# Performance work log

Measured on AMD Instinct MI355X. Metric: run time of the kernel, lower is better.

## Reference

```python
import jax, jax.numpy as jnp
import numpy as np

B, N, OBS, H, A = 4096, 32, 128, 64, 16

def setup_inputs() -> dict:
    key = jax.random.key(0)
    ks = jax.random.split(key, 12)
    s = 0.1  # weight scale for numerical stability
    return {
        "obs": jax.random.normal(ks[0], (B, N, OBS), jnp.float32),
        "enc_W": jax.random.normal(ks[1], (OBS, H), jnp.float32) * s,
        "enc_b": jnp.zeros((H,), jnp.float32),
        "msg_W0": jax.random.normal(ks[2], (H, H), jnp.float32) * s,
        "msg_b0": jnp.zeros((H,), jnp.float32),
        "msg_W1": jax.random.normal(ks[3], (H, H), jnp.float32) * s,
        "msg_b1": jnp.zeros((H,), jnp.float32),
        "lstm_Wx0": jax.random.normal(ks[4], (H, 4 * H), jnp.float32) * s,
        "lstm_Wh0": jax.random.normal(ks[5], (H, 4 * H), jnp.float32) * s,
        "lstm_b0": jnp.zeros((4 * H,), jnp.float32),
        "lstm_Wx1": jax.random.normal(ks[6], (H, 4 * H), jnp.float32) * s,
        "lstm_Wh1": jax.random.normal(ks[7], (H, 4 * H), jnp.float32) * s,
        "lstm_b1": jnp.zeros((4 * H,), jnp.float32),
        "act_W": jax.random.normal(ks[8], (H, A), jnp.float32) * s,
        "act_b": jnp.zeros((A,), jnp.float32),
        "val_W": jax.random.normal(ks[9], (H, 1), jnp.float32) * s,
        "val_b": jnp.zeros((1,), jnp.float32),
    }

def _lstm_cell(h, c, z, Wx, Wh, b):
    # flax OptimizedLSTMCell math: gates ordered i, f, g, o
    gates = z @ Wx + h @ Wh + b  # (BN, 4H)
    i, f, g, o = jnp.split(gates, 4, axis=-1)
    c_new = jax.nn.sigmoid(f) * c + jax.nn.sigmoid(i) * jnp.tanh(g)
    h_new = jax.nn.sigmoid(o) * jnp.tanh(c_new)
    return h_new, c_new

def reference(obs, enc_W, enc_b, msg_W0, msg_b0, msg_W1, msg_b1,
              lstm_Wx0, lstm_Wh0, lstm_b0, lstm_Wx1, lstm_Wh1, lstm_b1,
              act_W, act_b, val_W, val_b):
    b, n, _ = obs.shape
    x = jnp.tanh(obs @ enc_W + enc_b)  # (B, N, H)
    # carry=None -> zero initial state
    h_round = jnp.zeros((b, n, H), obs.dtype)
    c_round = jnp.zeros((b, n, H), obs.dtype)
    # alive_mask=None -> alive=ones(N); hard_attn=False -> no comm_action mask.
    # comm mixing matrix M[j, i] = comm_mask[j, i] * alive[j] * alive[i] / denom
    # with comm_mask = 1 - I and denom = max(num_alive - 1, 1) for 'avg' mode.
    denom = jnp.maximum(jnp.asarray(n, obs.dtype) - 1.0, 1.0)
    M = (jnp.ones((n, n), obs.dtype) - jnp.eye(n, dtype=obs.dtype)) / denom
    hop_params = [(msg_W0, msg_b0, lstm_Wx0, lstm_Wh0, lstm_b0),
                  (msg_W1, msg_b1, lstm_Wx1, lstm_Wh1, lstm_b1)]
    for (mW, mb, Wx, Wh, lb) in hop_params:
        # equivalent to broadcasting h to (B,N,N,H), masking, and summing over senders
        comm_sum = jnp.einsum('bjh,ji->bih', h_round, M)  # (B, N, H)
        msg = comm_sum @ mW + mb
        z = x + msg
        h_flat = h_round.reshape(b * n, H)
        c_flat = c_round.reshape(b * n, H)
        h_new, c_new = _lstm_cell(h_flat, c_flat, z.reshape(b * n, H), Wx, Wh, lb)
        h_round = jnp.tanh(h_new.reshape(b, n, H) + z)
        c_round = c_new.reshape(b, n, H)
    logits = h_round @ act_W + act_b           # (B, N, A)
    values = (h_round @ val_W + val_b)[..., 0]  # (B, N)
    return (logits, values, h_round, c_round)
```

## Files before the change

### kernel.cpp

```cpp
#include <hip/hip_runtime.h>
#include <hip/hip_bf16.h>

constexpr int Bn   = 4096;
constexpr int Nn   = 32;
constexpr int OBSn = 128;
constexpr int Hn   = 64;
constexpr int An   = 16;

constexpr size_t VOFF = (size_t)Bn * Nn * An;
constexpr size_t HOFF = VOFF + (size_t)Bn * Nn;
constexpr size_t COFF = HOFF + (size_t)Bn * Nn * Hn;

constexpr int T_ENC  = 0;
constexpr int T_MSG0 = 16;
constexpr int T_MSG1 = 24;
constexpr int T_WX0  = 32;
constexpr int T_WH0  = 64;
constexpr int T_WX1  = 96;
constexpr int T_WH1  = 128;
constexpr int T_ACT  = 160;
constexpr int T_TOT  = 162;

typedef short bf16x8 __attribute__((ext_vector_type(8)));
typedef float f32x4  __attribute__((ext_vector_type(4)));

union FragU { uint u[4]; uint4 q; bf16x8 v; };

__device__ __forceinline__ uint pkbf(float a, float b) {
    __hip_bfloat16 ha = __float2bfloat16(a);
    __hip_bfloat16 hb = __float2bfloat16(b);
    unsigned short ua, ub;
    __builtin_memcpy(&ua, &ha, 2);
    __builtin_memcpy(&ub, &hb, 2);
    return (uint)ua | ((uint)ub << 16);
}

__device__ __forceinline__ float rcp_(float x) {
#if __has_builtin(__builtin_amdgcn_rcpf)
    return __builtin_amdgcn_rcpf(x);
#else
    return 1.0f / x;
#endif
}
__device__ __forceinline__ float exp2_(float x) {
#if __has_builtin(__builtin_amdgcn_exp2f)
    return __builtin_amdgcn_exp2f(x);
#else
    return exp2f(x);
#endif
}
__device__ __forceinline__ float fsig(float x)  { return rcp_(1.0f + exp2_(-1.44269504f * x)); }
__device__ __forceinline__ float ftanh(float x) { return 1.0f - 2.0f * rcp_(1.0f + exp2_(2.88539008f * x)); }

__global__ void commnet_prep(
    const float* __restrict__ encW, const float* __restrict__ m0,
    const float* __restrict__ m1,   const float* __restrict__ wx0,
    const float* __restrict__ wh0,  const float* __restrict__ wx1,
    const float* __restrict__ wh1,  const float* __restrict__ aw,
    uint4* __restrict__ ws)
{
    int gid = blockIdx.x * 256 + threadIdx.x;
    if (gid >= T_TOT * 64) return;
    int tile = gid >> 6, lane = gid & 63;

    const float* W; int N, nt, kt, lt;
    if      (tile < T_MSG0) { W = encW; N = 64;  lt = tile;        nt = lt >> 2; kt = lt & 3; }
    else if (tile < T_MSG1) { W = m0;   N = 64;  lt = tile - T_MSG0; nt = lt >> 1; kt = lt & 1; }
    else if (tile < T_WX0 ) { W = m1;   N = 64;  lt = tile - T_MSG1; nt = lt >> 1; kt = lt & 1; }
    else if (tile < T_WH0 ) { W = wx0;  N = 256; lt = tile - T_WX0;  nt = lt >> 1; kt = lt & 1; }
    else if (tile < T_WX1 ) { W = wh0;  N = 256; lt = tile - T_WH0;  nt = lt >> 1; kt = lt & 1; }
    else if (tile < T_WH1 ) { W = wx1;  N = 256; lt = tile - T_WX1;  nt = lt >> 1; kt = lt & 1; }
    else if (tile < T_ACT ) { W = wh1;  N = 256; lt = tile - T_WH1;  nt = lt >> 1; kt = lt & 1; }
    else                    { W = aw;   N = 16;  lt = tile - T_ACT;  nt = 0;       kt = lt;     }

    int col = nt * 16 + (lane & 15);
    int kb  = kt * 32 + (lane >> 4) * 4;
    uint4 d;
    {
        int k0 = kb;
        d.x = pkbf(W[(k0 + 0) * N + col], W[(k0 + 1) * N + col]);
        d.y = pkbf(W[(k0 + 2) * N + col], W[(k0 + 3) * N + col]);
        k0 = kb + 16;
        d.z = pkbf(W[(k0 + 0) * N + col], W[(k0 + 1) * N + col]);
        d.w = pkbf(W[(k0 + 2) * N + col], W[(k0 + 3) * N + col]);
    }
    ws[(size_t)tile * 64 + lane] = d;
}

__device__ __forceinline__ int sidx(int row, int col) {
    return row * 64 + (col ^ ((row & 7) << 2));
}

__device__ __forceinline__ void write_cd(float* sb, const float v[2][4][4], int lane) {
    const int m = lane & 15, g = lane >> 4;
    #pragma unroll
    for (int rt = 0; rt < 2; ++rt)
        #pragma unroll
        for (int nt = 0; nt < 4; ++nt)
            #pragma unroll
            for (int r = 0; r < 4; ++r)
                sb[sidx(rt * 16 + g * 4 + r, nt * 16 + m)] = v[rt][nt][r];
}

__device__ __forceinline__ void read_af(const float* sb, int lane, FragU af[2][2]) {
    const int m = lane & 15, g = lane >> 4;
    #pragma unroll
    for (int rt = 0; rt < 2; ++rt)
        #pragma unroll
        for (int kt = 0; kt < 2; ++kt)
            #pragma unroll
            for (int h = 0; h < 2; ++h) {
                const float4 x = *(const float4*)&sb[sidx(rt * 16 + m, kt * 32 + h * 16 + g * 4)];
                af[rt][kt].u[2 * h]     = pkbf(x.x, x.y);
                af[rt][kt].u[2 * h + 1] = pkbf(x.z, x.w);
            }
}

template<bool WITHH>
__device__ __forceinline__ void gate_mm(const uint4* __restrict__ wsQ, int wxBase, int whBase,
                                        int gate, const FragU az[2][2], const FragU ah[2][2],
                                        const float* __restrict__ lb, int lane,
                                        float outv[2][4][4])
{
    const int m = lane & 15;
    #pragma unroll
    for (int nt = 0; nt < 4; ++nt) {
        f32x4 a0 = {0.f, 0.f, 0.f, 0.f};
        f32x4 a1 = {0.f, 0.f, 0.f, 0.f};
        const int ntg = gate * 4 + nt;
        #pragma unroll
        for (int kt = 0; kt < 2; ++kt) {
            FragU bw; bw.q = wsQ[(size_t)(wxBase + ntg * 2 + kt) * 64 + lane];
            a0 = __builtin_amdgcn_mfma_f32_16x16x32_bf16(az[0][kt].v, bw.v, a0, 0, 0, 0);
            a1 = __builtin_amdgcn_mfma_f32_16x16x32_bf16(az[1][kt].v, bw.v, a1, 0, 0, 0);
        }
        if (WITHH) {
            #pragma unroll
            for (int kt = 0; kt < 2; ++kt) {
                FragU bw; bw.q = wsQ[(size_t)(whBase + ntg * 2 + kt) * 64 + lane];
                a0 = __builtin_amdgcn_mfma_f32_16x16x32_bf16(ah[0][kt].v, bw.v, a0, 0, 0, 0);
                a1 = __builtin_amdgcn_mfma_f32_16x16x32_bf16(ah[1][kt].v, bw.v, a1, 0, 0, 0);
            }
        }
        const float lbv = lb[gate * 64 + nt * 16 + m];
        #pragma unroll
        for (int r = 0; r < 4; ++r) {
            outv[0][nt][r] = a0[r] + lbv;
            outv[1][nt][r] = a1[r] + lbv;
        }
    }
}

#define FORALL \
    _Pragma("unroll") for (int rt = 0; rt < 2; ++rt) \
    _Pragma("unroll") for (int nt = 0; nt < 4; ++nt) \
    _Pragma("unroll") for (int r = 0; r < 4; ++r)

__global__ __launch_bounds__(256, 2) void commnet_main(
    const float* __restrict__ obs, const uint4* __restrict__ wsQ,
    const float* __restrict__ enc_b,
    const float* __restrict__ msg_b0, const float* __restrict__ msg_b1,
    const float* __restrict__ lstm_b0, const float* __restrict__ lstm_b1,
    const float* __restrict__ act_b,
    const float* __restrict__ val_W, const float* __restrict__ val_b,
    float* __restrict__ out)
{
    __shared__ __align__(16) float sball[4 * 2048];
    const int t = threadIdx.x;
    const int wid = t >> 6, lane = t & 63;
    const int m = lane & 15, g = lane >> 4;
    float* sb = sball + wid * 2048;
    const int b = blockIdx.x * 4 + wid;

    FragU aob[2][4];
    const float* ob = obs + (size_t)b * (Nn * OBSn);
    #pragma unroll
    for (int rt = 0; rt < 2; ++rt)
        #pragma unroll
        for (int kt = 0; kt < 4; ++kt)
            #pragma unroll
            for (int h = 0; h < 2; ++h) {
                const float4 vv = *(const float4*)&ob[(rt * 16 + m) * OBSn + kt * 32 + h * 16 + g * 4];
                aob[rt][kt].u[2 * h]     = pkbf(vv.x, vv.y);
                aob[rt][kt].u[2 * h + 1] = pkbf(vv.z, vv.w);
            }
    float xv[2][4][4];
    #pragma unroll
    for (int nt = 0; nt < 4; ++nt) {
        f32x4 a0 = {0.f, 0.f, 0.f, 0.f};
        f32x4 a1 = {0.f, 0.f, 0.f, 0.f};
        #pragma unroll
        for (int kt = 0; kt < 4; ++kt) {
            FragU bw; bw.q = wsQ[(size_t)(T_ENC + nt * 4 + kt) * 64 + lane];
            a0 = __builtin_amdgcn_mfma_f32_16x16x32_bf16(aob[0][kt].v, bw.v, a0, 0, 0, 0);
            a1 = __builtin_amdgcn_mfma_f32_16x16x32_bf16(aob[1][kt].v, bw.v, a1, 0, 0, 0);
        }
        const float eb = enc_b[nt * 16 + m];
        #pragma unroll
        for (int r = 0; r < 4; ++r) {
            xv[0][nt][r] = ftanh(a0[r] + eb);
            xv[1][nt][r] = ftanh(a1[r] + eb);
        }
    }

    float zv[2][4][4], cv[2][4][4], hv[2][4][4], tg[2][4][4], si[2][4][4];
    FragU az[2][2], ah[2][2];

    #pragma unroll
    for (int nt = 0; nt < 4; ++nt) {
        const float mb = msg_b0[nt * 16 + m];
        #pragma unroll
        for (int rt = 0; rt < 2; ++rt)
            #pragma unroll
            for (int r = 0; r < 4; ++r)
                zv[rt][nt][r] = xv[rt][nt][r] + mb;
    }
    write_cd(sb, zv, lane);
    read_af(sb, lane, az);

    gate_mm<false>(wsQ, T_WX0, 0, 0, az, az, lstm_b0, lane, tg);
    FORALL { si[rt][nt][r] = fsig(tg[rt][nt][r]); }
    gate_mm<false>(wsQ, T_WX0, 0, 2, az, az, lstm_b0, lane, tg);
    FORALL { cv[rt][nt][r] = si[rt][nt][r] * ftanh(tg[rt][nt][r]); }
    gate_mm<false>(wsQ, T_WX0, 0, 3, az, az, lstm_b0, lane, tg);
    FORALL { hv[rt][nt][r] = ftanh(fsig(tg[rt][nt][r]) * ftanh(cv[rt][nt][r]) + zv[rt][nt][r]); }

    {
        float cm[2][4][4];
        #pragma unroll
        for (int nt = 0; nt < 4; ++nt) {
            float p = 0.f;
            #pragma unroll
            for (int rt = 0; rt < 2; ++rt)
                #pragma unroll
                for (int r = 0; r < 4; ++r) p += hv[rt][nt][r];
            p += __shfl_xor(p, 16);
            p += __shfl_xor(p, 32);
            #pragma unroll
            for (int rt = 0; rt < 2; ++rt)
                #pragma unroll
                for (int r = 0; r < 4; ++r)
                    cm[rt][nt][r] = (p - hv[rt][nt][r]) * (1.0f / 31.0f);
        }
        write_cd(sb, cm, lane);
        read_af(sb, lane, az);
    }
    #pragma unroll
    for (int nt = 0; nt < 4; ++nt) {
        f32x4 a0 = {0.f, 0.f, 0.f, 0.f};
        f32x4 a1 = {0.f, 0.f, 0.f, 0.f};
        #pragma unroll
        for (int kt = 0; kt < 2; ++kt) {
            FragU bw; bw.q = wsQ[(size_t)(T_MSG1 + nt * 2 + kt) * 64 + lane];
            a0 = __builtin_amdgcn_mfma_f32_16x16x32_bf16(az[0][kt].v, bw.v, a0, 0, 0, 0);
            a1 = __builtin_amdgcn_mfma_f32_16x16x32_bf16(az[1][kt].v, bw.v, a1, 0, 0, 0);
        }
        const float mb = msg_b1[nt * 16 + m];
        #pragma unroll
        for (int r = 0; r < 4; ++r) {
            zv[0][nt][r] = xv[0][nt][r] + a0[r] + mb;
            zv[1][nt][r] = xv[1][nt][r] + a1[r] + mb;
        }
    }
    write_cd(sb, zv, lane);
    read_af(sb, lane, az);
    write_cd(sb, hv, lane);
    read_af(sb, lane, ah);

    gate_mm<true>(wsQ, T_WX1, T_WH1, 1, az, ah, lstm_b1, lane, tg);
    FORALL { cv[rt][nt][r] = fsig(tg[rt][nt][r]) * cv[rt][nt][r]; }
    gate_mm<true>(wsQ, T_WX1, T_WH1, 0, az, ah, lstm_b1, lane, tg);
    FORALL { si[rt][nt][r] = fsig(tg[rt][nt][r]); }
    gate_mm<true>(wsQ, T_WX1, T_WH1, 2, az, ah, lstm_b1, lane, tg);
    FORALL { cv[rt][nt][r] = fmaf(si[rt][nt][r], ftanh(tg[rt][nt][r]), cv[rt][nt][r]); }
    gate_mm<true>(wsQ, T_WX1, T_WH1, 3, az, ah, lstm_b1, lane, tg);
    FORALL { hv[rt][nt][r] = ftanh(fsig(tg[rt][nt][r]) * ftanh(cv[rt][nt][r]) + zv[rt][nt][r]); }

    write_cd(sb, hv, lane);
    read_af(sb, lane, ah);
    {
        f32x4 l0 = {0.f, 0.f, 0.f, 0.f};
        f32x4 l1 = {0.f, 0.f, 0.f, 0.f};
        #pragma unroll
        for (int kt = 0; kt < 2; ++kt) {
            FragU bw; bw.q = wsQ[(size_t)(T_ACT + kt) * 64 + lane];
            l0 = __builtin_amdgcn_mfma_f32_16x16x32_bf16(ah[0][kt].v, bw.v, l0, 0, 0, 0);
            l1 = __builtin_amdgcn_mfma_f32_16x16x32_bf16(ah[1][kt].v, bw.v, l1, 0, 0, 0);
        }
        const float ab = act_b[m];
        #pragma unroll
        for (int r = 0; r < 4; ++r) {
            out[(size_t)(b * Nn +      g * 4 + r) * An + m] = l0[r] + ab;
            out[(size_t)(b * Nn + 16 + g * 4 + r) * An + m] = l1[r] + ab;
        }
    }
    {
        float vwv[4];
        #pragma unroll
        for (int nt = 0; nt < 4; ++nt) vwv[nt] = val_W[nt * 16 + m];
        const float vb = val_b[0];
        #pragma unroll
        for (int rt = 0; rt < 2; ++rt) {
            float p0 = 0.f, p1 = 0.f, p2 = 0.f, p3 = 0.f;
            #pragma unroll
            for (int nt = 0; nt < 4; ++nt) {
                p0 = fmaf(hv[rt][nt][0], vwv[nt], p0);
                p1 = fmaf(hv[rt][nt][1], vwv[nt], p1);
                p2 = fmaf(hv[rt][nt][2], vwv[nt], p2);
                p3 = fmaf(hv[rt][nt][3], vwv[nt], p3);
            }
            #pragma unroll
            for (int s = 1; s < 16; s <<= 1) {
                p0 += __shfl_xor(p0, s);
                p1 += __shfl_xor(p1, s);
                p2 += __shfl_xor(p2, s);
                p3 += __shfl_xor(p3, s);
            }
            float sel = (m == 0) ? p0 : (m == 1) ? p1 : (m == 2) ? p2 : p3;
            if (m < 4)
                out[VOFF + (size_t)b * Nn + rt * 16 + g * 4 + m] = sel + vb;
        }
    }
    {
        float* oh = out + HOFF;
        float* oc = out + COFF;
        FORALL {
            const size_t row = (size_t)b * Nn + rt * 16 + g * 4 + r;
            oh[row * Hn + nt * 16 + m] = hv[rt][nt][r];
            oc[row * Hn + nt * 16 + m] = cv[rt][nt][r];
        }
    }
}

extern "C" void kernel_launch(void* const* d_in, const int* in_sizes, int n_in,
                              void* d_out, int out_size, void* d_ws, size_t ws_size,
                              hipStream_t stream) {
    const float* obs      = (const float*)d_in[0];
    const float* enc_W    = (const float*)d_in[1];
    const float* enc_b    = (const float*)d_in[2];
    const float* msg_W0   = (const float*)d_in[3];
    const float* msg_b0   = (const float*)d_in[4];
    const float* msg_W1   = (const float*)d_in[5];
    const float* msg_b1   = (const float*)d_in[6];
    const float* lstm_Wx0 = (const float*)d_in[7];
    const float* lstm_Wh0 = (const float*)d_in[8];
    const float* lstm_b0  = (const float*)d_in[9];
    const float* lstm_Wx1 = (const float*)d_in[10];
    const float* lstm_Wh1 = (const float*)d_in[11];
    const float* lstm_b1  = (const float*)d_in[12];
    const float* act_W    = (const float*)d_in[13];
    const float* act_b    = (const float*)d_in[14];
    const float* val_W    = (const float*)d_in[15];
    const float* val_b    = (const float*)d_in[16];

    uint4* ws = (uint4*)d_ws;

    commnet_prep<<<(T_TOT * 64 + 255) / 256, 256, 0, stream>>>(
        enc_W, msg_W0, msg_W1, lstm_Wx0, lstm_Wh0, lstm_Wx1, lstm_Wh1, act_W, ws);

    commnet_main<<<Bn / 4, 256, 0, stream>>>(
        obs, ws, enc_b, msg_b0, msg_b1, lstm_b0, lstm_b1,
        act_b, val_W, val_b, (float*)d_out);
}
```

Baseline: 60.17 us.

## Swap MFMA operand order to keep activations in registers, drop LDS transposes

Computes each GEMM transposed (weights as the A operand, activations as the B operand), so the MFMA output layout matches the input fragment layout of the next GEMM. The per-wave shared-memory write/read transposes between stages can then be dropped, and state is packed to bf16 directly from registers. The output stores for h, c and logits also become 16-byte vector writes, and the comm-mean reduction uses in-row shuffles. This removes LDS traffic and latency on the dependent chain, but the shuffle pattern and store coalescing change.

```diff
diff --git a/kernel.cpp b/kernel.cpp
--- a/kernel.cpp
+++ b/kernel.cpp
@@ -51,6 +51,19 @@
 }
 __device__ __forceinline__ float fsig(float x)  { return rcp_(1.0f + exp2_(-1.44269504f * x)); }
 __device__ __forceinline__ float ftanh(float x) { return 1.0f - 2.0f * rcp_(1.0f + exp2_(2.88539008f * x)); }
+
+__device__ __forceinline__ f32x4 vsig(f32x4 x) {
+    f32x4 r;
+    #pragma unroll
+    for (int i = 0; i < 4; ++i) r[i] = fsig(x[i]);
+    return r;
+}
+__device__ __forceinline__ f32x4 vtanh(f32x4 x) {
+    f32x4 r;
+    #pragma unroll
+    for (int i = 0; i < 4; ++i) r[i] = ftanh(x[i]);
+    return r;
+}
 
 __global__ void commnet_prep(
     const float* __restrict__ encW, const float* __restrict__ m0,
@@ -87,74 +100,49 @@
     ws[(size_t)tile * 64 + lane] = d;
 }
 
-__device__ __forceinline__ int sidx(int row, int col) {
-    return row * 64 + (col ^ ((row & 7) << 2));
-}
-
-__device__ __forceinline__ void write_cd(float* sb, const float v[2][4][4], int lane) {
-    const int m = lane & 15, g = lane >> 4;
-    #pragma unroll
-    for (int rt = 0; rt < 2; ++rt)
-        #pragma unroll
-        for (int nt = 0; nt < 4; ++nt)
-            #pragma unroll
-            for (int r = 0; r < 4; ++r)
-                sb[sidx(rt * 16 + g * 4 + r, nt * 16 + m)] = v[rt][nt][r];
-}
-
-__device__ __forceinline__ void read_af(const float* sb, int lane, FragU af[2][2]) {
-    const int m = lane & 15, g = lane >> 4;
-    #pragma unroll
-    for (int rt = 0; rt < 2; ++rt)
-        #pragma unroll
-        for (int kt = 0; kt < 2; ++kt)
-            #pragma unroll
-            for (int h = 0; h < 2; ++h) {
-                const float4 x = *(const float4*)&sb[sidx(rt * 16 + m, kt * 32 + h * 16 + g * 4)];
-                af[rt][kt].u[2 * h]     = pkbf(x.x, x.y);
-                af[rt][kt].u[2 * h + 1] = pkbf(x.z, x.w);
-            }
+__device__ __forceinline__ void packState(const f32x4 v[2][4], FragU f[2][2]) {
+    #pragma unroll
+    for (int rt = 0; rt < 2; ++rt)
+        #pragma unroll
+        for (int p = 0; p < 2; ++p) {
+            f[rt][p].u[0] = pkbf(v[rt][2*p    ][0], v[rt][2*p    ][1]);
+            f[rt][p].u[1] = pkbf(v[rt][2*p    ][2], v[rt][2*p    ][3]);
+            f[rt][p].u[2] = pkbf(v[rt][2*p + 1][0], v[rt][2*p + 1][1]);
+            f[rt][p].u[3] = pkbf(v[rt][2*p + 1][2], v[rt][2*p + 1][3]);
+        }
 }
 
 template<bool WITHH>
 __device__ __forceinline__ void gate_mm(const uint4* __restrict__ wsQ, int wxBase, int whBase,
                                         int gate, const FragU az[2][2], const FragU ah[2][2],
                                         const float* __restrict__ lb, int lane,
-                                        float outv[2][4][4])
+                                        f32x4 outv[2][4])
 {
-    const int m = lane & 15;
+    const int g4 = (lane >> 4) * 4;
     #pragma unroll
     for (int nt = 0; nt < 4; ++nt) {
         f32x4 a0 = {0.f, 0.f, 0.f, 0.f};
         f32x4 a1 = {0.f, 0.f, 0.f, 0.f};
         const int ntg = gate * 4 + nt;
         #pragma unroll
-        for (int kt = 0; kt < 2; ++kt) {
-            FragU bw; bw.q = wsQ[(size_t)(wxBase + ntg * 2 + kt) * 64 + lane];
-            a0 = __builtin_amdgcn_mfma_f32_16x16x32_bf16(az[0][kt].v, bw.v, a0, 0, 0, 0);
-            a1 = __builtin_amdgcn_mfma_f32_16x16x32_bf16(az[1][kt].v, bw.v, a1, 0, 0, 0);
+        for (int p = 0; p < 2; ++p) {
+            FragU w; w.q = wsQ[(size_t)(wxBase + ntg * 2 + p) * 64 + lane];
+            a0 = __builtin_amdgcn_mfma_f32_16x16x32_bf16(w.v, az[0][p].v, a0, 0, 0, 0);
+            a1 = __builtin_amdgcn_mfma_f32_16x16x32_bf16(w.v, az[1][p].v, a1, 0, 0, 0);
         }
         if (WITHH) {
             #pragma unroll
-            for (int kt = 0; kt < 2; ++kt) {
-                FragU bw; bw.q = wsQ[(size_t)(whBase + ntg * 2 + kt) * 64 + lane];
-                a0 = __builtin_amdgcn_mfma_f32_16x16x32_bf16(ah[0][kt].v, bw.v, a0, 0, 0, 0);
-                a1 = __builtin_amdgcn_mfma_f32_16x16x32_bf16(ah[1][kt].v, bw.v, a1, 0, 0, 0);
+            for (int p = 0; p < 2; ++p) {
+                FragU w; w.q = wsQ[(size_t)(whBase + ntg * 2 + p) * 64 + lane];
+                a0 = __builtin_amdgcn_mfma_f32_16x16x32_bf16(w.v, ah[0][p].v, a0, 0, 0, 0);
+                a1 = __builtin_amdgcn_mfma_f32_16x16x32_bf16(w.v, ah[1][p].v, a1, 0, 0, 0);
             }
         }
-        const float lbv = lb[gate * 64 + nt * 16 + m];
-        #pragma unroll
-        for (int r = 0; r < 4; ++r) {
-            outv[0][nt][r] = a0[r] + lbv;
-            outv[1][nt][r] = a1[r] + lbv;
-        }
-    }
-}
-
-#define FORALL \
-    _Pragma("unroll") for (int rt = 0; rt < 2; ++rt) \
-    _Pragma("unroll") for (int nt = 0; nt < 4; ++nt) \
-    _Pragma("unroll") for (int r = 0; r < 4; ++r)
+        const f32x4 lbv = *(const f32x4*)&lb[gate * 64 + nt * 16 + g4];
+        outv[0][nt] = a0 + lbv;
+        outv[1][nt] = a1 + lbv;
+    }
+}
 
 __global__ __launch_bounds__(256, 2) void commnet_main(
     const float* __restrict__ obs, const uint4* __restrict__ wsQ,
@@ -165,170 +153,171 @@
     const float* __restrict__ val_W, const float* __restrict__ val_b,
     float* __restrict__ out)
 {
-    __shared__ __align__(16) float sball[4 * 2048];
     const int t = threadIdx.x;
     const int wid = t >> 6, lane = t & 63;
-    const int m = lane & 15, g = lane >> 4;
-    float* sb = sball + wid * 2048;
+    const int m = lane & 15, g4 = (lane >> 4) * 4;
     const int b = blockIdx.x * 4 + wid;
 
-    FragU aob[2][4];
+    FragU bo[2][4];
     const float* ob = obs + (size_t)b * (Nn * OBSn);
     #pragma unroll
     for (int rt = 0; rt < 2; ++rt)
         #pragma unroll
-        for (int kt = 0; kt < 4; ++kt)
-            #pragma unroll
-            for (int h = 0; h < 2; ++h) {
-                const float4 vv = *(const float4*)&ob[(rt * 16 + m) * OBSn + kt * 32 + h * 16 + g * 4];
-                aob[rt][kt].u[2 * h]     = pkbf(vv.x, vv.y);
-                aob[rt][kt].u[2 * h + 1] = pkbf(vv.z, vv.w);
-            }
-    float xv[2][4][4];
-    #pragma unroll
-    for (int nt = 0; nt < 4; ++nt) {
+        for (int kt = 0; kt < 4; ++kt) {
+            const float* p = &ob[(rt * 16 + m) * OBSn + kt * 32 + g4];
+            const f32x4 p0 = *(const f32x4*)p;
+            const f32x4 p1 = *(const f32x4*)(p + 16);
+            bo[rt][kt].u[0] = pkbf(p0[0], p0[1]);
+            bo[rt][kt].u[1] = pkbf(p0[2], p0[3]);
+            bo[rt][kt].u[2] = pkbf(p1[0], p1[1]);
+            bo[rt][kt].u[3] = pkbf(p1[2], p1[3]);
+        }
+
+    f32x4 xv[2][4], zv[2][4], cv[2][4], hv[2][4], tg[2][4], si[2][4];
+    FragU az[2][2], ah[2][2];
+
+    #pragma unroll
+    for (int ct = 0; ct < 4; ++ct) {
         f32x4 a0 = {0.f, 0.f, 0.f, 0.f};
         f32x4 a1 = {0.f, 0.f, 0.f, 0.f};
         #pragma unroll
         for (int kt = 0; kt < 4; ++kt) {
-            FragU bw; bw.q = wsQ[(size_t)(T_ENC + nt * 4 + kt) * 64 + lane];
-            a0 = __builtin_amdgcn_mfma_f32_16x16x32_bf16(aob[0][kt].v, bw.v, a0, 0, 0, 0);
-            a1 = __builtin_amdgcn_mfma_f32_16x16x32_bf16(aob[1][kt].v, bw.v, a1, 0, 0, 0);
-        }
-        const float eb = enc_b[nt * 16 + m];
-        #pragma unroll
-        for (int r = 0; r < 4; ++r) {
-            xv[0][nt][r] = ftanh(a0[r] + eb);
-            xv[1][nt][r] = ftanh(a1[r] + eb);
-        }
-    }
-
-    float zv[2][4][4], cv[2][4][4], hv[2][4][4], tg[2][4][4], si[2][4][4];
-    FragU az[2][2], ah[2][2];
-
-    #pragma unroll
-    for (int nt = 0; nt < 4; ++nt) {
-        const float mb = msg_b0[nt * 16 + m];
-        #pragma unroll
-        for (int rt = 0; rt < 2; ++rt)
-            #pragma unroll
-            for (int r = 0; r < 4; ++r)
-                zv[rt][nt][r] = xv[rt][nt][r] + mb;
-    }
-    write_cd(sb, zv, lane);
-    read_af(sb, lane, az);
+            FragU w; w.q = wsQ[(size_t)(T_ENC + ct * 4 + kt) * 64 + lane];
+            a0 = __builtin_amdgcn_mfma_f32_16x16x32_bf16(w.v, bo[0][kt].v, a0, 0, 0, 0);
+            a1 = __builtin_amdgcn_mfma_f32_16x16x32_bf16(w.v, bo[1][kt].v, a1, 0, 0, 0);
+        }
+        const f32x4 eb = *(const f32x4*)&enc_b[ct * 16 + g4];
+        xv[0][ct] = vtanh(a0 + eb);
+        xv[1][ct] = vtanh(a1 + eb);
+    }
+
+    #pragma unroll
+    for (int ct = 0; ct < 4; ++ct) {
+        const f32x4 mb = *(const f32x4*)&msg_b0[ct * 16 + g4];
+        zv[0][ct] = xv[0][ct] + mb;
+        zv[1][ct] = xv[1][ct] + mb;
+    }
+    packState(zv, az);
 
     gate_mm<false>(wsQ, T_WX0, 0, 0, az, az, lstm_b0, lane, tg);
-    FORALL { si[rt][nt][r] = fsig(tg[rt][nt][r]); }
+    #pragma unroll
+    for (int rt = 0; rt < 2; ++rt)
+        #pragma unroll
+        for (int ct = 0; ct < 4; ++ct) si[rt][ct] = vsig(tg[rt][ct]);
     gate_mm<false>(wsQ, T_WX0, 0, 2, az, az, lstm_b0, lane, tg);
-    FORALL { cv[rt][nt][r] = si[rt][nt][r] * ftanh(tg[rt][nt][r]); }
+    #pragma unroll
+    for (int rt = 0; rt < 2; ++rt)
+        #pragma unroll
+        for (int ct = 0; ct < 4; ++ct) cv[rt][ct] = si[rt][ct] * vtanh(tg[rt][ct]);
     gate_mm<false>(wsQ, T_WX0, 0, 3, az, az, lstm_b0, lane, tg);
-    FORALL { hv[rt][nt][r] = ftanh(fsig(tg[rt][nt][r]) * ftanh(cv[rt][nt][r]) + zv[rt][nt][r]); }
-
-    {
-        float cm[2][4][4];
-        #pragma unroll
-        for (int nt = 0; nt < 4; ++nt) {
-            float p = 0.f;
-            #pragma unroll
-            for (int rt = 0; rt < 2; ++rt)
-                #pragma unroll
-                for (int r = 0; r < 4; ++r) p += hv[rt][nt][r];
-            p += __shfl_xor(p, 16);
-            p += __shfl_xor(p, 32);
-            #pragma unroll
-            for (int rt = 0; rt < 2; ++rt)
+    #pragma unroll
+    for (int rt = 0; rt < 2; ++rt)
+        #pragma unroll
+        for (int ct = 0; ct < 4; ++ct)
+            hv[rt][ct] = vtanh(vsig(tg[rt][ct]) * vtanh(cv[rt][ct]) + zv[rt][ct]);
+
+    {
+        f32x4 cm[2][4];
+        #pragma unroll
+        for (int ct = 0; ct < 4; ++ct) {
+            f32x4 p = hv[0][ct] + hv[1][ct];
+            #pragma unroll
+            for (int r = 0; r < 4; ++r) {
+                float s = p[r];
+                s += __shfl_xor(s, 1);
+                s += __shfl_xor(s, 2);
+                s += __shfl_xor(s, 4);
+                s += __shfl_xor(s, 8);
+                p[r] = s;
+            }
+            cm[0][ct] = (p - hv[0][ct]) * (1.0f / 31.0f);
+            cm[1][ct] = (p - hv[1][ct]) * (1.0f / 31.0f);
+        }
+        packState(cm, az);
+    }
+    #pragma unroll
+    for (int ct = 0; ct < 4; ++ct) {
+        f32x4 a0 = {0.f, 0.f, 0.f, 0.f};
+        f32x4 a1 = {0.f, 0.f, 0.f, 0.f};
+        #pragma unroll
+        for (int p = 0; p < 2; ++p) {
+            FragU w; w.q = wsQ[(size_t)(T_MSG1 + ct * 2 + p) * 64 + lane];
+            a0 = __builtin_amdgcn_mfma_f32_16x16x32_bf16(w.v, az[0][p].v, a0, 0, 0, 0);
+            a1 = __builtin_amdgcn_mfma_f32_16x16x32_bf16(w.v, az[1][p].v, a1, 0, 0, 0);
+        }
+        const f32x4 mb = *(const f32x4*)&msg_b1[ct * 16 + g4];
+        zv[0][ct] = xv[0][ct] + a0 + mb;
+        zv[1][ct] = xv[1][ct] + a1 + mb;
+    }
+    packState(zv, az);
+    packState(hv, ah);
+
+    gate_mm<true>(wsQ, T_WX1, T_WH1, 1, az, ah, lstm_b1, lane, tg);
+    #pragma unroll
+    for (int rt = 0; rt < 2; ++rt)
+        #pragma unroll
+        for (int ct = 0; ct < 4; ++ct) cv[rt][ct] = vsig(tg[rt][ct]) * cv[rt][ct];
+    gate_mm<true>(wsQ, T_WX1, T_WH1, 0, az, ah, lstm_b1, lane, tg);
+    #pragma unroll
+    for (int rt = 0; rt < 2; ++rt)
+        #pragma unroll
+        for (int ct = 0; ct < 4; ++ct) si[rt][ct] = vsig(tg[rt][ct]);
+    gate_mm<true>(wsQ, T_WX1, T_WH1, 2, az, ah, lstm_b1, lane, tg);
+    #pragma unroll
+    for (int rt = 0; rt < 2; ++rt)
+        #pragma unroll
+        for (int ct = 0; ct < 4; ++ct) cv[rt][ct] = cv[rt][ct] + si[rt][ct] * vtanh(tg[rt][ct]);
+    gate_mm<true>(wsQ, T_WX1, T_WH1, 3, az, ah, lstm_b1, lane, tg);
+    #pragma unroll
+    for (int rt = 0; rt < 2; ++rt)
+        #pragma unroll
+        for (int ct = 0; ct < 4; ++ct)
+            hv[rt][ct] = vtanh(vsig(tg[rt][ct]) * vtanh(cv[rt][ct]) + zv[rt][ct]);
+
+    packState(hv, ah);
+    {
+        const f32x4 ab = *(const f32x4*)&act_b[g4];
+        #pragma unroll
+        for (int rt = 0; rt < 2; ++rt) {
+            f32x4 acc = {0.f, 0.f, 0.f, 0.f};
+            #pragma unroll
+            for (int p = 0; p < 2; ++p) {
+                FragU w; w.q = wsQ[(size_t)(T_ACT + p) * 64 + lane];
+                acc = __builtin_amdgcn_mfma_f32_16x16x32_bf16(w.v, ah[rt][p].v, acc, 0, 0, 0);
+            }
+            *(f32x4*)&out[((size_t)b * Nn + rt * 16 + m) * An + g4] = acc + ab;
+        }
+    }
+    {
+        const float vb = val_b[0];
+        f32x4 vw[4];
+        #pragma unroll
+        for (int ct = 0; ct < 4; ++ct) vw[ct] = *(const f32x4*)&val_W[ct * 16 + g4];
+        #pragma unroll
+        for (int rt = 0; rt < 2; ++rt) {
+            float pp = 0.f;
+            #pragma unroll
+            for (int ct = 0; ct < 4; ++ct)
                 #pragma unroll
                 for (int r = 0; r < 4; ++r)
-                    cm[rt][nt][r] = (p - hv[rt][nt][r]) * (1.0f / 31.0f);
-        }
-        write_cd(sb, cm, lane);
-        read_af(sb, lane, az);
-    }
-    #pragma unroll
-    for (int nt = 0; nt < 4; ++nt) {
-        f32x4 a0 = {0.f, 0.f, 0.f, 0.f};
-        f32x4 a1 = {0.f, 0.f, 0.f, 0.f};
-        #pragma unroll
-        for (int kt = 0; kt < 2; ++kt) {
-            FragU bw; bw.q = wsQ[(size_t)(T_MSG1 + nt * 2 + kt) * 64 + lane];
-            a0 = __builtin_amdgcn_mfma_f32_16x16x32_bf16(az[0][kt].v, bw.v, a0, 0, 0, 0);
-            a1 = __builtin_amdgcn_mfma_f32_16x16x32_bf16(az[1][kt].v, bw.v, a1, 0, 0, 0);
-        }
-        const float mb = msg_b1[nt * 16 + m];
-        #pragma unroll
-        for (int r = 0; r < 4; ++r) {
-            zv[0][nt][r] = xv[0][nt][r] + a0[r] + mb;
-            zv[1][nt][r] = xv[1][nt][r] + a1[r] + mb;
-        }
-    }
-    write_cd(sb, zv, lane);
-    read_af(sb, lane, az);
-    write_cd(sb, hv, lane);
-    read_af(sb, lane, ah);
-
-    gate_mm<true>(wsQ, T_WX1, T_WH1, 1, az, ah, lstm_b1, lane, tg);
-    FORALL { cv[rt][nt][r] = fsig(tg[rt][nt][r]) * cv[rt][nt][r]; }
-    gate_mm<true>(wsQ, T_WX1, T_WH1, 0, az, ah, lstm_b1, lane, tg);
-    FORALL { si[rt][nt][r] = fsig(tg[rt][nt][r]); }
-    gate_mm<true>(wsQ, T_WX1, T_WH1, 2, az, ah, lstm_b1, lane, tg);
-    FORALL { cv[rt][nt][r] = fmaf(si[rt][nt][r], ftanh(tg[rt][nt][r]), cv[rt][nt][r]); }
-    gate_mm<true>(wsQ, T_WX1, T_WH1, 3, az, ah, lstm_b1, lane, tg);
-    FORALL { hv[rt][nt][r] = ftanh(fsig(tg[rt][nt][r]) * ftanh(cv[rt][nt][r]) + zv[rt][nt][r]); }
-
-    write_cd(sb, hv, lane);
-    read_af(sb, lane, ah);
-    {
-        f32x4 l0 = {0.f, 0.f, 0.f, 0.f};
-        f32x4 l1 = {0.f, 0.f, 0.f, 0.f};
-        #pragma unroll
-        for (int kt = 0; kt < 2; ++kt) {
-            FragU bw; bw.q = wsQ[(size_t)(T_ACT + kt) * 64 + lane];
-            l0 = __builtin_amdgcn_mfma_f32_16x16x32_bf16(ah[0][kt].v, bw.v, l0, 0, 0, 0);
-            l1 = __builtin_amdgcn_mfma_f32_16x16x32_bf16(ah[1][kt].v, bw.v, l1, 0, 0, 0);
-        }
-        const float ab = act_b[m];
-        #pragma unroll
-        for (int r = 0; r < 4; ++r) {
-            out[(size_t)(b * Nn +      g * 4 + r) * An + m] = l0[r] + ab;
-            out[(size_t)(b * Nn + 16 + g * 4 + r) * An + m] = l1[r] + ab;
-        }
-    }
-    {
-        float vwv[4];
-        #pragma unroll
-        for (int nt = 0; nt < 4; ++nt) vwv[nt] = val_W[nt * 16 + m];
-        const float vb = val_b[0];
-        #pragma unroll
-        for (int rt = 0; rt < 2; ++rt) {
-            float p0 = 0.f, p1 = 0.f, p2 = 0.f, p3 = 0.f;
-            #pragma unroll
-            for (int nt = 0; nt < 4; ++nt) {
-                p0 = fmaf(hv[rt][nt][0], vwv[nt], p0);
-                p1 = fmaf(hv[rt][nt][1], vwv[nt], p1);
-                p2 = fmaf(hv[rt][nt][2], vwv[nt], p2);
-                p3 = fmaf(hv[rt][nt][3], vwv[nt], p3);
-            }
-            #pragma unroll
-            for (int s = 1; s < 16; s <<= 1) {
-                p0 += __shfl_xor(p0, s);
-                p1 += __shfl_xor(p1, s);
-                p2 += __shfl_xor(p2, s);
-                p3 += __shfl_xor(p3, s);
-            }
-            float sel = (m == 0) ? p0 : (m == 1) ? p1 : (m == 2) ? p2 : p3;
-            if (m < 4)
-                out[VOFF + (size_t)b * Nn + rt * 16 + g * 4 + m] = sel + vb;
+                    pp = fmaf(hv[rt][ct][r], vw[ct][r], pp);
+            pp += __shfl_xor(pp, 16);
+            pp += __shfl_xor(pp, 32);
+            if (g4 == 0)
+                out[VOFF + (size_t)b * Nn + rt * 16 + m] = pp + vb;
         }
     }
     {
         float* oh = out + HOFF;
         float* oc = out + COFF;
-        FORALL {
-            const size_t row = (size_t)b * Nn + rt * 16 + g * 4 + r;
-            oh[row * Hn + nt * 16 + m] = hv[rt][nt][r];
-            oc[row * Hn + nt * 16 + m] = cv[rt][nt][r];
-        }
+        #pragma unroll
+        for (int rt = 0; rt < 2; ++rt)
+            #pragma unroll
+            for (int ct = 0; ct < 4; ++ct) {
+                const size_t base = ((size_t)b * Nn + rt * 16 + m) * Hn + ct * 16 + g4;
+                *(f32x4*)&oh[base] = hv[rt][ct];
+                *(f32x4*)&oc[base] = cv[rt][ct];
+            }
     }
 }
 
```

Result: slower. 95.03 us (+57.9%).
